# Kernel tuning notes

Hardware: AMD Instinct MI355X
Metric: run time of the kernel (lower is better)

The kernel has to match this reference:

```python
import jax, jax.numpy as jnp
import numpy as np

N, E, F_IN, HID, EDIM = 20000, 320000, 16, 64, 1


def _add_self_loops(src, dst, eattr, n):
    # PyG add_self_loops with fill_value='mean': self-loop edge_attr = mean of
    # incoming edge_attr per destination node (0 if no incoming edges).
    deg = jax.ops.segment_sum(jnp.ones_like(eattr[:, 0]), dst, num_segments=n)
    mean_attr = jax.ops.segment_sum(eattr, dst, num_segments=n) / jnp.maximum(deg, 1.0)[:, None]
    loop = jnp.arange(n)
    return (jnp.concatenate([src, loop]), jnp.concatenate([dst, loop]),
            jnp.concatenate([eattr, mean_attr], axis=0))


def _gat_layer(x, src, dst, eattr, W, a_src, a_dst, We, a_e, b, heads, out_ch, n):
    # shared linear for src/dst (PyG GATConv with int in_channels)
    h = (x @ W).reshape(n, heads, out_ch)                      # [N,H,C]
    al_s = jnp.einsum('nhc,hc->nh', h, a_src)                  # [N,H]
    al_d = jnp.einsum('nhc,hc->nh', h, a_dst)
    ef = (eattr @ We).reshape(-1, heads, out_ch)               # [E,H,C]
    al_e = jnp.einsum('ehc,hc->eh', ef, a_e)                   # [E,H]
    alpha = jax.nn.leaky_relu(al_s[src] + al_d[dst] + al_e, 0.2)
    # segment softmax over destination node
    m = jax.ops.segment_max(alpha, dst, num_segments=n)
    m = jnp.where(jnp.isfinite(m), m, 0.0)
    ex = jnp.exp(alpha - m[dst])
    den = jax.ops.segment_sum(ex, dst, num_segments=n)
    coef = ex / (den[dst] + 1e-16)                             # [E,H]
    out = jax.ops.segment_sum(h[src] * coef[:, :, None], dst, num_segments=n)
    return out.reshape(n, heads * out_ch) + b


def setup_inputs() -> dict:
    key = jax.random.key(0)
    ks = jax.random.split(key, 24)
    s = 0.1
    inp = {
        'x': jax.random.normal(ks[0], (N, F_IN), jnp.float32),
        'edge_index': jax.random.randint(ks[1], (2, E), 0, N, jnp.int64),
        'edge_attr': jax.random.uniform(ks[2], (E, EDIM), jnp.float32),
        # layer 0: heads=4, in=16, out=64
        'W0': jax.random.normal(ks[3], (F_IN, 4 * HID), jnp.float32) * s,
        'as0': jax.random.normal(ks[4], (4, HID), jnp.float32) * s,
        'ad0': jax.random.normal(ks[5], (4, HID), jnp.float32) * s,
        'We0': jax.random.normal(ks[6], (EDIM, 4 * HID), jnp.float32) * s,
        'ae0': jax.random.normal(ks[7], (4, HID), jnp.float32) * s,
        'b0': jnp.zeros((4 * HID,), jnp.float32),
        # layer 1: heads=4, in=256, out=64
        'W1': jax.random.normal(ks[8], (4 * HID, 4 * HID), jnp.float32) * s,
        'as1': jax.random.normal(ks[9], (4, HID), jnp.float32) * s,
        'ad1': jax.random.normal(ks[10], (4, HID), jnp.float32) * s,
        'We1': jax.random.normal(ks[11], (EDIM, 4 * HID), jnp.float32) * s,
        'ae1': jax.random.normal(ks[12], (4, HID), jnp.float32) * s,
        'b1': jnp.zeros((4 * HID,), jnp.float32),
        # layer 2: heads=1, in=256, out=64
        'W2': jax.random.normal(ks[13], (4 * HID, HID), jnp.float32) * s,
        'as2': jax.random.normal(ks[14], (1, HID), jnp.float32) * s,
        'ad2': jax.random.normal(ks[15], (1, HID), jnp.float32) * s,
        'We2': jax.random.normal(ks[16], (EDIM, HID), jnp.float32) * s,
        'ae2': jax.random.normal(ks[17], (1, HID), jnp.float32) * s,
        'b2': jnp.zeros((HID,), jnp.float32),
        'ln_g': jnp.ones((HID,), jnp.float32),
        'ln_b': jnp.zeros((HID,), jnp.float32),
    }
    return inp


def reference(x, edge_index, edge_attr,
              W0, as0, ad0, We0, ae0, b0,
              W1, as1, ad1, We1, ae1, b1,
              W2, as2, ad2, We2, ae2, b2,
              ln_g, ln_b):
    n = x.shape[0]
    src, dst, eattr = _add_self_loops(edge_index[0], edge_index[1], edge_attr, n)
    h = _gat_layer(x, src, dst, eattr, W0, as0, ad0, We0, ae0, b0, 4, HID, n)
    h = jax.nn.elu(h)  # dropout is identity in eval
    h = _gat_layer(h, src, dst, eattr, W1, as1, ad1, We1, ae1, b1, 4, HID, n)
    h = jax.nn.elu(h)
    h = _gat_layer(h, src, dst, eattr, W2, as2, ad2, We2, ae2, b2, 1, HID, n)
    mu = jnp.mean(h, axis=-1, keepdims=True)
    var = jnp.mean((h - mu) ** 2, axis=-1, keepdims=True)
    return (h - mu) / jnp.sqrt(var + 1e-5) * ln_g + ln_b
```

## Files before the change

kernel.cpp:

```cpp
#include <hip/hip_runtime.h>
#include <hip/hip_bf16.h>
#include <math.h>


typedef __attribute__((ext_vector_type(8))) short short8;
typedef __attribute__((ext_vector_type(4))) float float4v;

#define CAP 64

__device__ __forceinline__ float wave_sum(float v) {
#pragma unroll
  for (int off = 32; off > 0; off >>= 1) v += __shfl_xor(v, off, 64);
  return v;
}

__device__ __forceinline__ unsigned short f2bf(float v) {
  unsigned u = __float_as_uint(v);
  unsigned r = u + 0x7fff + ((u >> 16) & 1);
  return (unsigned short)(r >> 16);
}

__device__ __forceinline__ float bf2f(unsigned short u) {
  return __uint_as_float(((unsigned)u) << 16);
}

__global__ __launch_bounds__(256) void k1_kernel(
    const float* __restrict__ x, const int* __restrict__ srcv, const int* __restrict__ dstv,
    const float* __restrict__ eattr,
    const float* __restrict__ W0, const float* __restrict__ as0, const float* __restrict__ ad0,
    const float* __restrict__ We0, const float* __restrict__ ae0,
    const float* __restrict__ W1, const float* __restrict__ as1, const float* __restrict__ ad1,
    const float* __restrict__ We1, const float* __restrict__ ae1,
    const float* __restrict__ W2, const float* __restrict__ as2, const float* __restrict__ ad2,
    const float* __restrict__ We2, const float* __restrict__ ae2,
    unsigned short* __restrict__ Wf1, unsigned short* __restrict__ Wf2,
    float* __restrict__ wedot, float* __restrict__ al_s, float* __restrict__ al_d,
    int* __restrict__ deg, int2* __restrict__ ebuf,
    int N, int E, int gD) {
  int b = blockIdx.x;
  int tid = threadIdx.x;
  if (b < 272) {
    int idx = b * 256 + tid;
    int j = idx & 7, lane = (idx >> 3) & 63, ks = (idx >> 9) & 7, nt = idx >> 12;
    int k = ks * 32 + (lane >> 4) * 8 + j;
    int col = lane & 15;
    float v = 0.f;
    if (nt < 16) {
      v = W1[(size_t)k * 256 + nt * 16 + col];
    } else if (col < 4) {
      for (int c = 0; c < 64; c++) v = fmaf(W1[(size_t)k * 256 + col * 64 + c], as1[col * 64 + c], v);
    } else if (col < 8) {
      int h = col - 4;
      for (int c = 0; c < 64; c++) v = fmaf(W1[(size_t)k * 256 + h * 64 + c], ad1[h * 64 + c], v);
    }
    Wf1[idx] = f2bf(v);
  } else if (b < 352) {
    int idx = (b - 272) * 256 + tid;
    int j = idx & 7, lane = (idx >> 3) & 63, ks = (idx >> 9) & 7, nt = idx >> 12;
    int k = ks * 32 + (lane >> 4) * 8 + j;
    int col = lane & 15;
    float v = 0.f;
    if (nt < 4) {
      v = W2[(size_t)k * 64 + nt * 16 + col];
    } else if (col < 1) {
      for (int c = 0; c < 64; c++) v = fmaf(W2[(size_t)k * 64 + c], as2[c], v);
    } else if (col < 2) {
      for (int c = 0; c < 64; c++) v = fmaf(W2[(size_t)k * 64 + c], ad2[c], v);
    }
    Wf2[idx] = f2bf(v);
  } else if (b == 352) {
    if (tid >= 64) return;
    int c = tid;
    for (int h = 0; h < 4; h++) {
      float v = wave_sum(We0[h * 64 + c] * ae0[h * 64 + c]);
      if (c == 0) wedot[h] = v;
    }
    for (int h = 0; h < 4; h++) {
      float v = wave_sum(We1[h * 64 + c] * ae1[h * 64 + c]);
      if (c == 0) wedot[4 + h] = v;
    }
    float v = wave_sum(We2[c] * ae2[c]);
    if (c == 0) wedot[8] = v;
  } else if (b < 353 + gD) {
    __shared__ float va[128];
    if (tid < 128) {
      int k = tid >> 3, col = tid & 7;
      float v = 0.f;
      if (col < 4) {
        for (int c = 0; c < 64; c++) v = fmaf(W0[(size_t)k * 256 + col * 64 + c], as0[col * 64 + c], v);
      } else {
        int h = col - 4;
        for (int c = 0; c < 64; c++) v = fmaf(W0[(size_t)k * 256 + h * 64 + c], ad0[h * 64 + c], v);
      }
      va[tid] = v;
    }
    __syncthreads();
    int node = (b - 353) * 256 + tid;
    if (node >= N) return;
    const float4* xr = (const float4*)(x + (size_t)node * 16);
    float4 xv[4];
#pragma unroll
    for (int q = 0; q < 4; q++) xv[q] = xr[q];
    float al[8];
#pragma unroll
    for (int j = 0; j < 8; j++) al[j] = 0.f;
#pragma unroll
    for (int k = 0; k < 16; k++) {
      float xk = ((const float*)xv)[k];
#pragma unroll
      for (int j = 0; j < 8; j++) al[j] = fmaf(xk, va[k * 8 + j], al[j]);
    }
    ((float4*)al_s)[node] = make_float4(al[0], al[1], al[2], al[3]);
    ((float4*)al_d)[node] = make_float4(al[4], al[5], al[6], al[7]);
  } else {
    int e = (b - 353 - gD) * 256 + tid;
    if (e >= E) return;
    int d = dstv[e];
    int s = srcv[e];
    float ea = eattr[e];
    int pos = atomicAdd(&deg[d], 1);
    if (pos < CAP) ebuf[(size_t)d * CAP + pos] = make_int2(s, __float_as_int(ea));
  }
}

__global__ __launch_bounds__(256) void agg0_kernel(
    const int* __restrict__ deg, const int2* __restrict__ ebuf,
    const float* __restrict__ al_s, const float* __restrict__ al_d,
    const float* __restrict__ wedot,
    const float* __restrict__ x, const float* __restrict__ W0,
    const float* __restrict__ bias, unsigned short* __restrict__ out, int n) {
  int node = blockIdx.x * 4 + (threadIdx.x >> 6);
  if (node >= n) return;
  int lane = threadIdx.x & 63;
  int es = lane >> 4;
  int c = lane & 15;
  int dg = deg[node];
  int cnt = dg < CAP ? dg : CAP;
  float xself = x[(size_t)node * 16 + c];
  float4 as4s = ((const float4*)al_s)[node];
  float4 ald = ((const float4*)al_d)[node];
  float wd[4];
#pragma unroll
  for (int h = 0; h < 4; h++) wd[h] = wedot[h];

  float Z[4] = {0.f, 0.f, 0.f, 0.f};
  float den[4] = {0.f, 0.f, 0.f, 0.f};
  float easum = 0.f;

  for (int i = 0; i < cnt; i += 4) {
    int base = __builtin_amdgcn_readfirstlane(node * CAP + i);
    int2 r0 = ebuf[base], r1 = ebuf[base + 1], r2 = ebuf[base + 2], r3 = ebuf[base + 3];
    int2 rm = (es == 0) ? r0 : (es == 1) ? r1 : (es == 2) ? r2 : r3;
    bool valid = (i + es) < cnt;
    int src = valid ? rm.x : 0;
    float ev = valid ? __int_as_float(rm.y) : 0.f;
    float xv = x[(size_t)src * 16 + c];
    float4 as4 = ((const float4*)al_s)[src];
    easum += ev;
#pragma unroll
    for (int h = 0; h < 4; h++) {
      float a = ((const float*)&as4)[h] + ((const float*)&ald)[h] + ev * wd[h];
      a = fmaxf(a, 0.2f * a);
      a = fminf(a, 30.f);
      float wv = __expf(a);
      wv = valid ? wv : 0.f;
      den[h] += wv;
      Z[h] = fmaf(wv, xv, Z[h]);
    }
  }

#pragma unroll
  for (int h = 0; h < 4; h++) {
    Z[h] += __shfl_xor(Z[h], 16, 64);
    Z[h] += __shfl_xor(Z[h], 32, 64);
    den[h] += __shfl_xor(den[h], 16, 64);
    den[h] += __shfl_xor(den[h], 32, 64);
  }
  easum += __shfl_xor(easum, 16, 64);
  easum += __shfl_xor(easum, 32, 64);

  {
    float evs = easum / fmaxf((float)dg, 1.f);
#pragma unroll
    for (int h = 0; h < 4; h++) {
      float a = ((const float*)&as4s)[h] + ((const float*)&ald)[h] + evs * wd[h];
      a = fmaxf(a, 0.2f * a);
      a = fminf(a, 30.f);
      float wv = __expf(a);
      den[h] += wv;
      Z[h] = fmaf(wv, xself, Z[h]);
    }
  }

  int h = es;
  float zsel = (h == 0) ? Z[0] : (h == 1) ? Z[1] : (h == 2) ? Z[2] : Z[3];
  float dsel = (h == 0) ? den[0] : (h == 1) ? den[1] : (h == 2) ? den[2] : den[3];
  float zn = zsel / (dsel + 1e-16f);
  float4 w0r[16];
#pragma unroll
  for (int cc = 0; cc < 16; cc++) w0r[cc] = ((const float4*)(W0 + (size_t)cc * 256))[lane];
  float zc[16];
  int basel = lane & 48;
#pragma unroll
  for (int cc = 0; cc < 16; cc++) zc[cc] = __shfl(zn, basel + cc, 64);
  float o[4];
  float4 b4 = ((const float4*)bias)[lane];
#pragma unroll
  for (int jj = 0; jj < 4; jj++) o[jj] = ((const float*)&b4)[jj];
#pragma unroll
  for (int cc = 0; cc < 16; cc++) {
#pragma unroll
    for (int jj = 0; jj < 4; jj++) o[jj] = fmaf(zc[cc], ((const float*)&w0r[cc])[jj], o[jj]);
  }
  ushort4 o4;
  float ox = o[0] > 0.f ? o[0] : expm1f(o[0]);
  float oy = o[1] > 0.f ? o[1] : expm1f(o[1]);
  float oz = o[2] > 0.f ? o[2] : expm1f(o[2]);
  float ow = o[3] > 0.f ? o[3] : expm1f(o[3]);
  o4.x = f2bf(ox);
  o4.y = f2bf(oy);
  o4.z = f2bf(oz);
  o4.w = f2bf(ow);
  ((ushort4*)out)[(size_t)node * 64 + lane] = o4;
}

template <int M, int H>
__global__ __launch_bounds__(64) void mfma_gemm_dots(
    const unsigned short* __restrict__ Abf, const unsigned short* __restrict__ Wfrag,
    unsigned short* __restrict__ out, float* __restrict__ al_s, float* __restrict__ al_d,
    int n) {
  int lane = threadIdx.x;
  int row0 = blockIdx.x * 16;
  int m = lane & 15, q = lane >> 4;

  short8 afrag[8];
  int r = row0 + m;
  if (r < n) {
    const short8* arow = (const short8*)(Abf + (size_t)r * 256);
#pragma unroll
    for (int ks = 0; ks < 8; ks++) afrag[ks] = arow[ks * 4 + q];
  } else {
#pragma unroll
    for (int ks = 0; ks < 8; ks++) afrag[ks] = (short8)0;
  }

  const short8* wf = (const short8*)Wfrag;

  auto epi = [&](int tile, float4v acc) {
    int col = tile * 16 + m;
#pragma unroll
    for (int reg = 0; reg < 4; reg++) {
      int rr = row0 + q * 4 + reg;
      if (rr < n) out[(size_t)rr * M + col] = f2bf(acc[reg]);
    }
  };

  for (int nt = 0; nt < M / 16; nt += 2) {
    const short8* b0 = wf + (size_t)nt * 8 * 64 + lane;
    const short8* b1 = b0 + 8 * 64;
    short8 bf0[8], bf1[8];
#pragma unroll
    for (int ks = 0; ks < 8; ks++) {
      bf0[ks] = b0[ks * 64];
      bf1[ks] = b1[ks * 64];
    }
    float4v acc0 = {0.f, 0.f, 0.f, 0.f};
    float4v acc1 = {0.f, 0.f, 0.f, 0.f};
#pragma unroll
    for (int ks = 0; ks < 8; ks++) {
      acc0 = __builtin_amdgcn_mfma_f32_16x16x32_bf16(afrag[ks], bf0[ks], acc0, 0, 0, 0);
      acc1 = __builtin_amdgcn_mfma_f32_16x16x32_bf16(afrag[ks], bf1[ks], acc1, 0, 0, 0);
    }
    epi(nt, acc0);
    epi(nt + 1, acc1);
  }

  {
    const short8* bl = wf + (size_t)(M / 16) * 8 * 64 + lane;
    short8 bf[8];
#pragma unroll
    for (int ks = 0; ks < 8; ks++) bf[ks] = bl[ks * 64];
    float4v acc = {0.f, 0.f, 0.f, 0.f};
#pragma unroll
    for (int ks = 0; ks < 8; ks++)
      acc = __builtin_amdgcn_mfma_f32_16x16x32_bf16(afrag[ks], bf[ks], acc, 0, 0, 0);
#pragma unroll
    for (int reg = 0; reg < 4; reg++) {
      int rr = row0 + q * 4 + reg;
      if (rr < n) {
        if (m < H) al_s[(size_t)rr * H + m] = acc[reg];
        else if (m < 2 * H) al_d[(size_t)rr * H + (m - H)] = acc[reg];
      }
    }
  }
}

__global__ __launch_bounds__(256) void agg4_kernel(
    const int* __restrict__ deg, const int2* __restrict__ ebuf,
    const float* __restrict__ al_s, const float* __restrict__ al_d,
    const float* __restrict__ wedot,
    const unsigned short* __restrict__ B, const float* __restrict__ bias,
    unsigned short* __restrict__ out, int n) {
  int node = blockIdx.x * 4 + (threadIdx.x >> 6);
  if (node >= n) return;
  int lane = threadIdx.x & 63;
  int half = lane >> 5;
  int l = lane & 31;
  int h4 = l >> 3;
  int dg = deg[node];
  int cnt = dg < CAP ? dg : CAP;
  float aldh = al_d[(size_t)node * 4 + h4];
  float alsh = al_s[(size_t)node * 4 + h4];
  float wdh = wedot[h4];
  short8 rowS = ((const short8*)(B + (size_t)node * 256))[l];

  float acc[8];
#pragma unroll
  for (int j = 0; j < 8; j++) acc[j] = 0.f;
  float den = 0.f;
  float easum = 0.f;

  for (int i = 0; i < cnt; i += 4) {
    int base = __builtin_amdgcn_readfirstlane(node * CAP + i);
    int2 r0 = ebuf[base], r1 = ebuf[base + 1], r2 = ebuf[base + 2], r3 = ebuf[base + 3];
    bool vA = (i + (half ? 1 : 0)) < cnt;
    bool vB = (i + (half ? 3 : 2)) < cnt;
    int2 rA = half ? r1 : r0;
    int2 rB = half ? r3 : r2;
    int srcA = vA ? rA.x : 0;
    int srcB = vB ? rB.x : 0;
    float evA = vA ? __int_as_float(rA.y) : 0.f;
    float evB = vB ? __int_as_float(rB.y) : 0.f;
    easum += evA + evB;
    float aA = al_s[(size_t)srcA * 4 + h4] + aldh + evA * wdh;
    float aB = al_s[(size_t)srcB * 4 + h4] + aldh + evB * wdh;
    aA = fmaxf(aA, 0.2f * aA);
    aB = fmaxf(aB, 0.2f * aB);
    aA = fminf(aA, 30.f);
    aB = fminf(aB, 30.f);
    float wA = __expf(aA);
    float wB = __expf(aB);
    wA = vA ? wA : 0.f;
    wB = vB ? wB : 0.f;
    short8 rowA = ((const short8*)(B + (size_t)srcA * 256))[l];
    short8 rowB = ((const short8*)(B + (size_t)srcB * 256))[l];
    den += wA + wB;
    const unsigned short* pa = (const unsigned short*)&rowA;
    const unsigned short* pb = (const unsigned short*)&rowB;
#pragma unroll
    for (int j = 0; j < 8; j++) acc[j] = fmaf(wA, bf2f(pa[j]), acc[j]);
#pragma unroll
    for (int j = 0; j < 8; j++) acc[j] = fmaf(wB, bf2f(pb[j]), acc[j]);
  }

  den += __shfl_xor(den, 32, 64);
  easum += __shfl_xor(easum, 32, 64);
#pragma unroll
  for (int j = 0; j < 8; j++) acc[j] += __shfl_xor(acc[j], 32, 64);

  {
    float evs = easum / fmaxf((float)dg, 1.f);
    float a = alsh + aldh + evs * wdh;
    a = fmaxf(a, 0.2f * a);
    a = fminf(a, 30.f);
    float wv = __expf(a);
    const unsigned short* ps = (const unsigned short*)&rowS;
    den += wv;
#pragma unroll
    for (int j = 0; j < 8; j++) acc[j] = fmaf(wv, bf2f(ps[j]), acc[j]);
  }

  if (half == 0) {
    float inv = 1.f / (den + 1e-16f);
    float4 b0 = ((const float4*)bias)[l * 2];
    float4 b1 = ((const float4*)bias)[l * 2 + 1];
    unsigned short o8[8];
#pragma unroll
    for (int j = 0; j < 8; j++) {
      float bjv = (j < 4) ? ((const float*)&b0)[j] : ((const float*)&b1)[j - 4];
      float o = acc[j] * inv + bjv;
      o = o > 0.f ? o : expm1f(o);
      o8[j] = f2bf(o);
    }
    ((short8*)(out + (size_t)node * 256))[l] = *(short8*)o8;
  }
}

__global__ __launch_bounds__(256) void agg_ln_kernel(
    const int* __restrict__ deg, const int2* __restrict__ ebuf,
    const float* __restrict__ al_s, const float* __restrict__ al_d,
    const float* __restrict__ wedot,
    const unsigned short* __restrict__ B, const float* __restrict__ bias,
    const float* __restrict__ ln_g, const float* __restrict__ ln_b,
    float* __restrict__ out, int n) {
  int node = blockIdx.x * 4 + (threadIdx.x >> 6);
  if (node >= n) return;
  int lane = threadIdx.x & 63;
  int q = lane >> 4;
  int l = lane & 15;
  int dg = deg[node];
  int cnt = dg < CAP ? dg : CAP;
  float ald = al_d[node];
  float als = al_s[node];
  float wd = wedot[0];
  ushort4 bvS = ((const ushort4*)(B + (size_t)node * 64))[l];

  float4 acc = make_float4(0.f, 0.f, 0.f, 0.f);
  float den = 0.f;
  float easum = 0.f;

  for (int i = 0; i < cnt; i += 4) {
    int base = __builtin_amdgcn_readfirstlane(node * CAP + i);
    int2 r0 = ebuf[base], r1 = ebuf[base + 1], r2 = ebuf[base + 2], r3 = ebuf[base + 3];
    int2 rm = (q == 0) ? r0 : (q == 1) ? r1 : (q == 2) ? r2 : r3;
    bool valid = (i + q) < cnt;
    int src = valid ? rm.x : 0;
    float ev = valid ? __int_as_float(rm.y) : 0.f;
    easum += ev;
    float a = al_s[src] + ald + ev * wd;
    a = fmaxf(a, 0.2f * a);
    a = fminf(a, 30.f);
    float wv = __expf(a);
    wv = valid ? wv : 0.f;
    ushort4 bv = ((const ushort4*)(B + (size_t)src * 64))[l];
    den += wv;
    acc.x = fmaf(wv, bf2f(bv.x), acc.x);
    acc.y = fmaf(wv, bf2f(bv.y), acc.y);
    acc.z = fmaf(wv, bf2f(bv.z), acc.z);
    acc.w = fmaf(wv, bf2f(bv.w), acc.w);
  }

  den += __shfl_xor(den, 32, 64);
  den += __shfl_xor(den, 16, 64);
  easum += __shfl_xor(easum, 32, 64);
  easum += __shfl_xor(easum, 16, 64);
  acc.x += __shfl_xor(acc.x, 32, 64);
  acc.y += __shfl_xor(acc.y, 32, 64);
  acc.z += __shfl_xor(acc.z, 32, 64);
  acc.w += __shfl_xor(acc.w, 32, 64);
  acc.x += __shfl_xor(acc.x, 16, 64);
  acc.y += __shfl_xor(acc.y, 16, 64);
  acc.z += __shfl_xor(acc.z, 16, 64);
  acc.w += __shfl_xor(acc.w, 16, 64);

  {
    float evs = easum / fmaxf((float)dg, 1.f);
    float a = als + ald + evs * wd;
    a = fmaxf(a, 0.2f * a);
    a = fminf(a, 30.f);
    float wv = __expf(a);
    den += wv;
    acc.x = fmaf(wv, bf2f(bvS.x), acc.x);
    acc.y = fmaf(wv, bf2f(bvS.y), acc.y);
    acc.z = fmaf(wv, bf2f(bvS.z), acc.z);
    acc.w = fmaf(wv, bf2f(bvS.w), acc.w);
  }

  float inv = 1.f / (den + 1e-16f);
  float4 b4 = ((const float4*)bias)[l];
  float4 o;
  o.x = acc.x * inv + b4.x;
  o.y = acc.y * inv + b4.y;
  o.z = acc.z * inv + b4.z;
  o.w = acc.w * inv + b4.w;
  float s = (o.x + o.y) + (o.z + o.w);
#pragma unroll
  for (int off = 1; off < 16; off <<= 1) s += __shfl_xor(s, off, 64);
  float mu = s * (1.f / 64.f);
  float dx = o.x - mu, dy = o.y - mu, dz = o.z - mu, dw = o.w - mu;
  float v = (dx * dx + dy * dy) + (dz * dz + dw * dw);
#pragma unroll
  for (int off = 1; off < 16; off <<= 1) v += __shfl_xor(v, off, 64);
  float rs = rsqrtf(v * (1.f / 64.f) + 1e-5f);
  if (q == 0) {
    float4 g4 = ((const float4*)ln_g)[l];
    float4 lb4 = ((const float4*)ln_b)[l];
    float4 rr;
    rr.x = dx * rs * g4.x + lb4.x;
    rr.y = dy * rs * g4.y + lb4.y;
    rr.z = dz * rs * g4.z + lb4.z;
    rr.w = dw * rs * g4.w + lb4.w;
    ((float4*)(out + (size_t)node * 64))[l] = rr;
  }
}

extern "C" void kernel_launch(void* const* d_in, const int* in_sizes, int n_in,
                              void* d_out, int out_size, void* d_ws, size_t ws_size,
                              hipStream_t stream) {
  const float* x = (const float*)d_in[0];
  const int* ei = (const int*)d_in[1];
  const float* eattr = (const float*)d_in[2];
  const float* W0 = (const float*)d_in[3];
  const float* as0 = (const float*)d_in[4];
  const float* ad0 = (const float*)d_in[5];
  const float* We0 = (const float*)d_in[6];
  const float* ae0 = (const float*)d_in[7];
  const float* b0 = (const float*)d_in[8];
  const float* W1 = (const float*)d_in[9];
  const float* as1 = (const float*)d_in[10];
  const float* ad1 = (const float*)d_in[11];
  const float* We1 = (const float*)d_in[12];
  const float* ae1 = (const float*)d_in[13];
  const float* b1 = (const float*)d_in[14];
  const float* W2 = (const float*)d_in[15];
  const float* as2 = (const float*)d_in[16];
  const float* ad2 = (const float*)d_in[17];
  const float* We2 = (const float*)d_in[18];
  const float* ae2 = (const float*)d_in[19];
  const float* b2 = (const float*)d_in[20];
  const float* lng = (const float*)d_in[21];
  const float* lnb = (const float*)d_in[22];
  float* outp = (float*)d_out;

  const int N = in_sizes[0] / 16;
  const int E = in_sizes[1] / 2;
  const int* srcv = ei;
  const int* dstv = ei + E;

  char* w = (char*)d_ws;
  size_t off = 0;
  auto alloc = [&](size_t bytes) -> void* {
    void* p = w + off;
    off += (bytes + 255) & ~(size_t)255;
    return p;
  };
  int* deg = (int*)alloc((size_t)N * 4);
  size_t zero_bytes = off;
  int2* ebuf = (int2*)alloc(((size_t)N * CAP + 8) * 8);
  float* wedot = (float*)alloc(16 * 4);
  float* al_s = (float*)alloc((size_t)N * 4 * 4);
  float* al_d = (float*)alloc((size_t)N * 4 * 4);
  unsigned short* Wf1 = (unsigned short*)alloc((size_t)17 * 4096 * 2);
  unsigned short* Wf2 = (unsigned short*)alloc((size_t)5 * 4096 * 2);
  unsigned short* bufA = (unsigned short*)alloc((size_t)N * 256 * 2);
  unsigned short* bufB = (unsigned short*)alloc((size_t)N * 256 * 2);
  (void)ws_size;

  hipMemsetAsync(d_ws, 0, zero_bytes, stream);

  int gE = (E + 255) / 256;
  int gD = (N + 255) / 256;

  k1_kernel<<<353 + gD + gE, 256, 0, stream>>>(
      x, srcv, dstv, eattr, W0, as0, ad0, We0, ae0, W1, as1, ad1, We1, ae1,
      W2, as2, ad2, We2, ae2, Wf1, Wf2, wedot, al_s, al_d, deg, ebuf, N, E, gD);

  int gStrip = (N + 15) / 16;
  int gNode4 = (N + 3) / 4;

  agg0_kernel<<<gNode4, 256, 0, stream>>>(deg, ebuf, al_s, al_d, wedot, x, W0, b0,
                                          bufA, N);

  mfma_gemm_dots<256, 4><<<gStrip, 64, 0, stream>>>(bufA, Wf1, bufB, al_s, al_d, N);
  agg4_kernel<<<gNode4, 256, 0, stream>>>(deg, ebuf, al_s, al_d, wedot + 4, bufB, b1,
                                          bufA, N);

  mfma_gemm_dots<64, 1><<<gStrip, 64, 0, stream>>>(bufA, Wf2, bufB, al_s, al_d, N);
  agg_ln_kernel<<<gNode4, 256, 0, stream>>>(deg, ebuf, al_s, al_d, wedot + 8, bufB, b2,
                                            lng, lnb, outp, N);
}
```

Before: 215.1 us.

## Fuse per-layer aggregation with following MFMA GEMM through shared-memory row tiles

Each aggregation kernel now processes a 16-node tile: four waves each aggregate four nodes, write the bf16 activated rows into shared memory, then the block runs the next layer's MFMA projection (including the attention-dot columns) straight from LDS. This removes two kernel launches and the global write and re-read of the intermediate 256-wide activation buffer. It also gives each layer its own attention-score buffers so a fused kernel never overwrites scores it is still reading. In exchange, each block handles nodes serially per wave, which lowers parallelism and can add tail imbalance when degrees vary.

```diff
diff --git a/kernel.cpp b/kernel.cpp
--- a/kernel.cpp
+++ b/kernel.cpp
@@ -34,7 +34,7 @@
     const float* __restrict__ W2, const float* __restrict__ as2, const float* __restrict__ ad2,
     const float* __restrict__ We2, const float* __restrict__ ae2,
     unsigned short* __restrict__ Wf1, unsigned short* __restrict__ Wf2,
-    float* __restrict__ wedot, float* __restrict__ al_s, float* __restrict__ al_d,
+    float* __restrict__ wedot, float* __restrict__ al0s, float* __restrict__ al0d,
     int* __restrict__ deg, int2* __restrict__ ebuf,
     int N, int E, int gD) {
   int b = blockIdx.x;
@@ -110,8 +110,8 @@
 #pragma unroll
       for (int j = 0; j < 8; j++) al[j] = fmaf(xk, va[k * 8 + j], al[j]);
     }
-    ((float4*)al_s)[node] = make_float4(al[0], al[1], al[2], al[3]);
-    ((float4*)al_d)[node] = make_float4(al[4], al[5], al[6], al[7]);
+    ((float4*)al0s)[node] = make_float4(al[0], al[1], al[2], al[3]);
+    ((float4*)al0d)[node] = make_float4(al[4], al[5], al[6], al[7]);
   } else {
     int e = (b - 353 - gD) * 256 + tid;
     if (e >= E) return;
@@ -123,160 +123,128 @@
   }
 }
 
-__global__ __launch_bounds__(256) void agg0_kernel(
+__global__ __launch_bounds__(256) void fused0_kernel(
     const int* __restrict__ deg, const int2* __restrict__ ebuf,
-    const float* __restrict__ al_s, const float* __restrict__ al_d,
+    const float* __restrict__ al0s, const float* __restrict__ al0d,
     const float* __restrict__ wedot,
     const float* __restrict__ x, const float* __restrict__ W0,
-    const float* __restrict__ bias, unsigned short* __restrict__ out, int n) {
-  int node = blockIdx.x * 4 + (threadIdx.x >> 6);
-  if (node >= n) return;
+    const float* __restrict__ b0, const unsigned short* __restrict__ Wf1,
+    unsigned short* __restrict__ buf256, float* __restrict__ al1s,
+    float* __restrict__ al1d, int n) {
+  __shared__ unsigned short hrow[16][264];
+  int tile = blockIdx.x;
+  int wv = threadIdx.x >> 6;
   int lane = threadIdx.x & 63;
   int es = lane >> 4;
   int c = lane & 15;
-  int dg = deg[node];
-  int cnt = dg < CAP ? dg : CAP;
-  float xself = x[(size_t)node * 16 + c];
-  float4 as4s = ((const float4*)al_s)[node];
-  float4 ald = ((const float4*)al_d)[node];
-  float wd[4];
-#pragma unroll
-  for (int h = 0; h < 4; h++) wd[h] = wedot[h];
-
-  float Z[4] = {0.f, 0.f, 0.f, 0.f};
-  float den[4] = {0.f, 0.f, 0.f, 0.f};
-  float easum = 0.f;
-
-  for (int i = 0; i < cnt; i += 4) {
-    int base = __builtin_amdgcn_readfirstlane(node * CAP + i);
-    int2 r0 = ebuf[base], r1 = ebuf[base + 1], r2 = ebuf[base + 2], r3 = ebuf[base + 3];
-    int2 rm = (es == 0) ? r0 : (es == 1) ? r1 : (es == 2) ? r2 : r3;
-    bool valid = (i + es) < cnt;
-    int src = valid ? rm.x : 0;
-    float ev = valid ? __int_as_float(rm.y) : 0.f;
-    float xv = x[(size_t)src * 16 + c];
-    float4 as4 = ((const float4*)al_s)[src];
-    easum += ev;
-#pragma unroll
-    for (int h = 0; h < 4; h++) {
-      float a = ((const float*)&as4)[h] + ((const float*)&ald)[h] + ev * wd[h];
-      a = fmaxf(a, 0.2f * a);
-      a = fminf(a, 30.f);
-      float wv = __expf(a);
-      wv = valid ? wv : 0.f;
-      den[h] += wv;
-      Z[h] = fmaf(wv, xv, Z[h]);
-    }
-  }
-
-#pragma unroll
-  for (int h = 0; h < 4; h++) {
-    Z[h] += __shfl_xor(Z[h], 16, 64);
-    Z[h] += __shfl_xor(Z[h], 32, 64);
-    den[h] += __shfl_xor(den[h], 16, 64);
-    den[h] += __shfl_xor(den[h], 32, 64);
-  }
-  easum += __shfl_xor(easum, 16, 64);
-  easum += __shfl_xor(easum, 32, 64);
-
-  {
-    float evs = easum / fmaxf((float)dg, 1.f);
-#pragma unroll
-    for (int h = 0; h < 4; h++) {
-      float a = ((const float*)&as4s)[h] + ((const float*)&ald)[h] + evs * wd[h];
-      a = fmaxf(a, 0.2f * a);
-      a = fminf(a, 30.f);
-      float wv = __expf(a);
-      den[h] += wv;
-      Z[h] = fmaf(wv, xself, Z[h]);
-    }
-  }
-
-  int h = es;
-  float zsel = (h == 0) ? Z[0] : (h == 1) ? Z[1] : (h == 2) ? Z[2] : Z[3];
-  float dsel = (h == 0) ? den[0] : (h == 1) ? den[1] : (h == 2) ? den[2] : den[3];
-  float zn = zsel / (dsel + 1e-16f);
-  float4 w0r[16];
-#pragma unroll
-  for (int cc = 0; cc < 16; cc++) w0r[cc] = ((const float4*)(W0 + (size_t)cc * 256))[lane];
-  float zc[16];
-  int basel = lane & 48;
-#pragma unroll
-  for (int cc = 0; cc < 16; cc++) zc[cc] = __shfl(zn, basel + cc, 64);
-  float o[4];
-  float4 b4 = ((const float4*)bias)[lane];
-#pragma unroll
-  for (int jj = 0; jj < 4; jj++) o[jj] = ((const float*)&b4)[jj];
-#pragma unroll
-  for (int cc = 0; cc < 16; cc++) {
-#pragma unroll
-    for (int jj = 0; jj < 4; jj++) o[jj] = fmaf(zc[cc], ((const float*)&w0r[cc])[jj], o[jj]);
-  }
-  ushort4 o4;
-  float ox = o[0] > 0.f ? o[0] : expm1f(o[0]);
-  float oy = o[1] > 0.f ? o[1] : expm1f(o[1]);
-  float oz = o[2] > 0.f ? o[2] : expm1f(o[2]);
-  float ow = o[3] > 0.f ? o[3] : expm1f(o[3]);
-  o4.x = f2bf(ox);
-  o4.y = f2bf(oy);
-  o4.z = f2bf(oz);
-  o4.w = f2bf(ow);
-  ((ushort4*)out)[(size_t)node * 64 + lane] = o4;
-}
-
-template <int M, int H>
-__global__ __launch_bounds__(64) void mfma_gemm_dots(
-    const unsigned short* __restrict__ Abf, const unsigned short* __restrict__ Wfrag,
-    unsigned short* __restrict__ out, float* __restrict__ al_s, float* __restrict__ al_d,
-    int n) {
-  int lane = threadIdx.x;
-  int row0 = blockIdx.x * 16;
+
+  for (int s = 0; s < 4; s++) {
+    int r = wv * 4 + s;
+    int node = tile * 16 + r;
+    if (node < n) {
+      int dg = deg[node];
+      int cnt = dg < CAP ? dg : CAP;
+      float xself = x[(size_t)node * 16 + c];
+      float4 as4s = ((const float4*)al0s)[node];
+      float4 ald = ((const float4*)al0d)[node];
+      float wd[4];
+#pragma unroll
+      for (int h = 0; h < 4; h++) wd[h] = wedot[h];
+
+      float Z[4] = {0.f, 0.f, 0.f, 0.f};
+      float den[4] = {0.f, 0.f, 0.f, 0.f};
+      float easum = 0.f;
+
+      for (int i = 0; i < cnt; i += 4) {
+        int base = __builtin_amdgcn_readfirstlane(node * CAP + i);
+        int2 r0 = ebuf[base], r1 = ebuf[base + 1], r2 = ebuf[base + 2], r3 = ebuf[base + 3];
+        int2 rm = (es == 0) ? r0 : (es == 1) ? r1 : (es == 2) ? r2 : r3;
+        bool valid = (i + es) < cnt;
+        int src = valid ? rm.x : 0;
+        float ev = valid ? __int_as_float(rm.y) : 0.f;
+        float xv = x[(size_t)src * 16 + c];
+        float4 as4 = ((const float4*)al0s)[src];
+        easum += ev;
+#pragma unroll
+        for (int h = 0; h < 4; h++) {
+          float a = ((const float*)&as4)[h] + ((const float*)&ald)[h] + ev * wd[h];
+          a = fmaxf(a, 0.2f * a);
+          a = fminf(a, 30.f);
+          float wvv = __expf(a);
+          wvv = valid ? wvv : 0.f;
+          den[h] += wvv;
+          Z[h] = fmaf(wvv, xv, Z[h]);
+        }
+      }
+
+#pragma unroll
+      for (int h = 0; h < 4; h++) {
+        Z[h] += __shfl_xor(Z[h], 16, 64);
+        Z[h] += __shfl_xor(Z[h], 32, 64);
+        den[h] += __shfl_xor(den[h], 16, 64);
+        den[h] += __shfl_xor(den[h], 32, 64);
+      }
+      easum += __shfl_xor(easum, 16, 64);
+      easum += __shfl_xor(easum, 32, 64);
+
+      {
+        float evs = easum / fmaxf((float)dg, 1.f);
+#pragma unroll
+        for (int h = 0; h < 4; h++) {
+          float a = ((const float*)&as4s)[h] + ((const float*)&ald)[h] + evs * wd[h];
+          a = fmaxf(a, 0.2f * a);
+          a = fminf(a, 30.f);
+          float wvv = __expf(a);
+          den[h] += wvv;
+          Z[h] = fmaf(wvv, xself, Z[h]);
+        }
+      }
+
+      int h = es;
+      float zsel = (h == 0) ? Z[0] : (h == 1) ? Z[1] : (h == 2) ? Z[2] : Z[3];
+      float dsel = (h == 0) ? den[0] : (h == 1) ? den[1] : (h == 2) ? den[2] : den[3];
+      float zn = zsel / (dsel + 1e-16f);
+      float4 w0r[16];
+#pragma unroll
+      for (int cc = 0; cc < 16; cc++) w0r[cc] = ((const float4*)(W0 + (size_t)cc * 256))[lane];
+      float zc[16];
+      int basel = lane & 48;
+#pragma unroll
+      for (int cc = 0; cc < 16; cc++) zc[cc] = __shfl(zn, basel + cc, 64);
+      float o[4];
+      float4 b4 = ((const float4*)b0)[lane];
+#pragma unroll
+      for (int jj = 0; jj < 4; jj++) o[jj] = ((const float*)&b4)[jj];
+#pragma unroll
+      for (int cc = 0; cc < 16; cc++) {
+#pragma unroll
+        for (int jj = 0; jj < 4; jj++) o[jj] = fmaf(zc[cc], ((const float*)&w0r[cc])[jj], o[jj]);
+      }
+      ushort4 o4;
+      float ox = o[0] > 0.f ? o[0] : expm1f(o[0]);
+      float oy = o[1] > 0.f ? o[1] : expm1f(o[1]);
+      float oz = o[2] > 0.f ? o[2] : expm1f(o[2]);
+      float ow = o[3] > 0.f ? o[3] : expm1f(o[3]);
+      o4.x = f2bf(ox);
+      o4.y = f2bf(oy);
+      o4.z = f2bf(oz);
+      o4.w = f2bf(ow);
+      *(ushort4*)&hrow[r][lane * 4] = o4;
+    } else {
+      *(ushort4*)&hrow[r][lane * 4] = make_ushort4(0, 0, 0, 0);
+    }
+  }
+  __syncthreads();
+
   int m = lane & 15, q = lane >> 4;
-
+  int row0 = tile * 16;
   short8 afrag[8];
-  int r = row0 + m;
-  if (r < n) {
-    const short8* arow = (const short8*)(Abf + (size_t)r * 256);
-#pragma unroll
-    for (int ks = 0; ks < 8; ks++) afrag[ks] = arow[ks * 4 + q];
-  } else {
-#pragma unroll
-    for (int ks = 0; ks < 8; ks++) afrag[ks] = (short8)0;
-  }
-
-  const short8* wf = (const short8*)Wfrag;
-
-  auto epi = [&](int tile, float4v acc) {
-    int col = tile * 16 + m;
-#pragma unroll
-    for (int reg = 0; reg < 4; reg++) {
-      int rr = row0 + q * 4 + reg;
-      if (rr < n) out[(size_t)rr * M + col] = f2bf(acc[reg]);
-    }
-  };
-
-  for (int nt = 0; nt < M / 16; nt += 2) {
-    const short8* b0 = wf + (size_t)nt * 8 * 64 + lane;
-    const short8* b1 = b0 + 8 * 64;
-    short8 bf0[8], bf1[8];
-#pragma unroll
-    for (int ks = 0; ks < 8; ks++) {
-      bf0[ks] = b0[ks * 64];
-      bf1[ks] = b1[ks * 64];
-    }
-    float4v acc0 = {0.f, 0.f, 0.f, 0.f};
-    float4v acc1 = {0.f, 0.f, 0.f, 0.f};
-#pragma unroll
-    for (int ks = 0; ks < 8; ks++) {
-      acc0 = __builtin_amdgcn_mfma_f32_16x16x32_bf16(afrag[ks], bf0[ks], acc0, 0, 0, 0);
-      acc1 = __builtin_amdgcn_mfma_f32_16x16x32_bf16(afrag[ks], bf1[ks], acc1, 0, 0, 0);
-    }
-    epi(nt, acc0);
-    epi(nt + 1, acc1);
-  }
-
-  {
-    const short8* bl = wf + (size_t)(M / 16) * 8 * 64 + lane;
+#pragma unroll
+  for (int ks = 0; ks < 8; ks++) afrag[ks] = *(short8*)&hrow[m][ks * 32 + q * 8];
+
+  const short8* wf = (const short8*)Wf1;
+  for (int nt = wv; nt < 17; nt += 4) {
+    const short8* bl = wf + (size_t)nt * 8 * 64 + lane;
     short8 bf[8];
 #pragma unroll
     for (int ks = 0; ks < 8; ks++) bf[ks] = bl[ks * 64];
@@ -284,111 +252,168 @@
 #pragma unroll
     for (int ks = 0; ks < 8; ks++)
       acc = __builtin_amdgcn_mfma_f32_16x16x32_bf16(afrag[ks], bf[ks], acc, 0, 0, 0);
-#pragma unroll
-    for (int reg = 0; reg < 4; reg++) {
-      int rr = row0 + q * 4 + reg;
-      if (rr < n) {
-        if (m < H) al_s[(size_t)rr * H + m] = acc[reg];
-        else if (m < 2 * H) al_d[(size_t)rr * H + (m - H)] = acc[reg];
-      }
-    }
-  }
-}
-
-__global__ __launch_bounds__(256) void agg4_kernel(
+    if (nt < 16) {
+      int col = nt * 16 + m;
+#pragma unroll
+      for (int reg = 0; reg < 4; reg++) {
+        int rr = row0 + q * 4 + reg;
+        if (rr < n) buf256[(size_t)rr * 256 + col] = f2bf(acc[reg]);
+      }
+    } else {
+#pragma unroll
+      for (int reg = 0; reg < 4; reg++) {
+        int rr = row0 + q * 4 + reg;
+        if (rr < n) {
+          if (m < 4) al1s[(size_t)rr * 4 + m] = acc[reg];
+          else if (m < 8) al1d[(size_t)rr * 4 + (m - 4)] = acc[reg];
+        }
+      }
+    }
+  }
+}
+
+__global__ __launch_bounds__(256) void fused1_kernel(
     const int* __restrict__ deg, const int2* __restrict__ ebuf,
-    const float* __restrict__ al_s, const float* __restrict__ al_d,
+    const float* __restrict__ al1s, const float* __restrict__ al1d,
     const float* __restrict__ wedot,
-    const unsigned short* __restrict__ B, const float* __restrict__ bias,
-    unsigned short* __restrict__ out, int n) {
-  int node = blockIdx.x * 4 + (threadIdx.x >> 6);
-  if (node >= n) return;
+    const unsigned short* __restrict__ buf256, const float* __restrict__ b1,
+    const unsigned short* __restrict__ Wf2, unsigned short* __restrict__ buf64,
+    float* __restrict__ al2s, float* __restrict__ al2d, int n) {
+  __shared__ unsigned short hrow[16][264];
+  int tile = blockIdx.x;
+  int wv = threadIdx.x >> 6;
   int lane = threadIdx.x & 63;
   int half = lane >> 5;
   int l = lane & 31;
   int h4 = l >> 3;
-  int dg = deg[node];
-  int cnt = dg < CAP ? dg : CAP;
-  float aldh = al_d[(size_t)node * 4 + h4];
-  float alsh = al_s[(size_t)node * 4 + h4];
-  float wdh = wedot[h4];
-  short8 rowS = ((const short8*)(B + (size_t)node * 256))[l];
-
-  float acc[8];
-#pragma unroll
-  for (int j = 0; j < 8; j++) acc[j] = 0.f;
-  float den = 0.f;
-  float easum = 0.f;
-
-  for (int i = 0; i < cnt; i += 4) {
-    int base = __builtin_amdgcn_readfirstlane(node * CAP + i);
-    int2 r0 = ebuf[base], r1 = ebuf[base + 1], r2 = ebuf[base + 2], r3 = ebuf[base + 3];
-    bool vA = (i + (half ? 1 : 0)) < cnt;
-    bool vB = (i + (half ? 3 : 2)) < cnt;
-    int2 rA = half ? r1 : r0;
-    int2 rB = half ? r3 : r2;
-    int srcA = vA ? rA.x : 0;
-    int srcB = vB ? rB.x : 0;
-    float evA = vA ? __int_as_float(rA.y) : 0.f;
-    float evB = vB ? __int_as_float(rB.y) : 0.f;
-    easum += evA + evB;
-    float aA = al_s[(size_t)srcA * 4 + h4] + aldh + evA * wdh;
-    float aB = al_s[(size_t)srcB * 4 + h4] + aldh + evB * wdh;
-    aA = fmaxf(aA, 0.2f * aA);
-    aB = fmaxf(aB, 0.2f * aB);
-    aA = fminf(aA, 30.f);
-    aB = fminf(aB, 30.f);
-    float wA = __expf(aA);
-    float wB = __expf(aB);
-    wA = vA ? wA : 0.f;
-    wB = vB ? wB : 0.f;
-    short8 rowA = ((const short8*)(B + (size_t)srcA * 256))[l];
-    short8 rowB = ((const short8*)(B + (size_t)srcB * 256))[l];
-    den += wA + wB;
-    const unsigned short* pa = (const unsigned short*)&rowA;
-    const unsigned short* pb = (const unsigned short*)&rowB;
-#pragma unroll
-    for (int j = 0; j < 8; j++) acc[j] = fmaf(wA, bf2f(pa[j]), acc[j]);
-#pragma unroll
-    for (int j = 0; j < 8; j++) acc[j] = fmaf(wB, bf2f(pb[j]), acc[j]);
-  }
-
-  den += __shfl_xor(den, 32, 64);
-  easum += __shfl_xor(easum, 32, 64);
-#pragma unroll
-  for (int j = 0; j < 8; j++) acc[j] += __shfl_xor(acc[j], 32, 64);
-
-  {
-    float evs = easum / fmaxf((float)dg, 1.f);
-    float a = alsh + aldh + evs * wdh;
-    a = fmaxf(a, 0.2f * a);
-    a = fminf(a, 30.f);
-    float wv = __expf(a);
-    const unsigned short* ps = (const unsigned short*)&rowS;
-    den += wv;
-#pragma unroll
-    for (int j = 0; j < 8; j++) acc[j] = fmaf(wv, bf2f(ps[j]), acc[j]);
-  }
-
-  if (half == 0) {
-    float inv = 1.f / (den + 1e-16f);
-    float4 b0 = ((const float4*)bias)[l * 2];
-    float4 b1 = ((const float4*)bias)[l * 2 + 1];
-    unsigned short o8[8];
-#pragma unroll
-    for (int j = 0; j < 8; j++) {
-      float bjv = (j < 4) ? ((const float*)&b0)[j] : ((const float*)&b1)[j - 4];
-      float o = acc[j] * inv + bjv;
-      o = o > 0.f ? o : expm1f(o);
-      o8[j] = f2bf(o);
-    }
-    ((short8*)(out + (size_t)node * 256))[l] = *(short8*)o8;
+
+  for (int s = 0; s < 4; s++) {
+    int r = wv * 4 + s;
+    int node = tile * 16 + r;
+    if (node < n) {
+      int dg = deg[node];
+      int cnt = dg < CAP ? dg : CAP;
+      float aldh = al1d[(size_t)node * 4 + h4];
+      float alsh = al1s[(size_t)node * 4 + h4];
+      float wdh = wedot[4 + h4];
+      short8 rowS = ((const short8*)(buf256 + (size_t)node * 256))[l];
+
+      float acc[8];
+#pragma unroll
+      for (int j = 0; j < 8; j++) acc[j] = 0.f;
+      float den = 0.f;
+      float easum = 0.f;
+
+      for (int i = 0; i < cnt; i += 4) {
+        int base = __builtin_amdgcn_readfirstlane(node * CAP + i);
+        int2 r0 = ebuf[base], r1 = ebuf[base + 1], r2 = ebuf[base + 2], r3 = ebuf[base + 3];
+        bool vA = (i + (half ? 1 : 0)) < cnt;
+        bool vB = (i + (half ? 3 : 2)) < cnt;
+        int2 rA = half ? r1 : r0;
+        int2 rB = half ? r3 : r2;
+        int srcA = vA ? rA.x : 0;
+        int srcB = vB ? rB.x : 0;
+        float evA = vA ? __int_as_float(rA.y) : 0.f;
+        float evB = vB ? __int_as_float(rB.y) : 0.f;
+        easum += evA + evB;
+        float aA = al1s[(size_t)srcA * 4 + h4] + aldh + evA * wdh;
+        float aB = al1s[(size_t)srcB * 4 + h4] + aldh + evB * wdh;
+        aA = fmaxf(aA, 0.2f * aA);
+        aB = fmaxf(aB, 0.2f * aB);
+        aA = fminf(aA, 30.f);
+        aB = fminf(aB, 30.f);
+        float wA = __expf(aA);
+        float wB = __expf(aB);
+        wA = vA ? wA : 0.f;
+        wB = vB ? wB : 0.f;
+        short8 rowA = ((const short8*)(buf256 + (size_t)srcA * 256))[l];
+        short8 rowB = ((const short8*)(buf256 + (size_t)srcB * 256))[l];
+        den += wA + wB;
+        const unsigned short* pa = (const unsigned short*)&rowA;
+        const unsigned short* pb = (const unsigned short*)&rowB;
+#pragma unroll
+        for (int j = 0; j < 8; j++) acc[j] = fmaf(wA, bf2f(pa[j]), acc[j]);
+#pragma unroll
+        for (int j = 0; j < 8; j++) acc[j] = fmaf(wB, bf2f(pb[j]), acc[j]);
+      }
+
+      den += __shfl_xor(den, 32, 64);
+      easum += __shfl_xor(easum, 32, 64);
+#pragma unroll
+      for (int j = 0; j < 8; j++) acc[j] += __shfl_xor(acc[j], 32, 64);
+
+      {
+        float evs = easum / fmaxf((float)dg, 1.f);
+        float a = alsh + aldh + evs * wdh;
+        a = fmaxf(a, 0.2f * a);
+        a = fminf(a, 30.f);
+        float wvv = __expf(a);
+        const unsigned short* ps = (const unsigned short*)&rowS;
+        den += wvv;
+#pragma unroll
+        for (int j = 0; j < 8; j++) acc[j] = fmaf(wvv, bf2f(ps[j]), acc[j]);
+      }
+
+      if (half == 0) {
+        float inv = 1.f / (den + 1e-16f);
+        float4 bb0 = ((const float4*)b1)[l * 2];
+        float4 bb1 = ((const float4*)b1)[l * 2 + 1];
+        unsigned short o8[8];
+#pragma unroll
+        for (int j = 0; j < 8; j++) {
+          float bjv = (j < 4) ? ((const float*)&bb0)[j] : ((const float*)&bb1)[j - 4];
+          float o = acc[j] * inv + bjv;
+          o = o > 0.f ? o : expm1f(o);
+          o8[j] = f2bf(o);
+        }
+        *(short8*)&hrow[r][l * 8] = *(short8*)o8;
+      }
+    } else if (half == 0) {
+      unsigned short z8[8] = {0, 0, 0, 0, 0, 0, 0, 0};
+      *(short8*)&hrow[r][l * 8] = *(short8*)z8;
+    }
+  }
+  __syncthreads();
+
+  int m = lane & 15, q = lane >> 4;
+  int row0 = tile * 16;
+  short8 afrag[8];
+#pragma unroll
+  for (int ks = 0; ks < 8; ks++) afrag[ks] = *(short8*)&hrow[m][ks * 32 + q * 8];
+
+  const short8* wf = (const short8*)Wf2;
+  for (int nt = wv; nt < 5; nt += 4) {
+    const short8* bl = wf + (size_t)nt * 8 * 64 + lane;
+    short8 bf[8];
+#pragma unroll
+    for (int ks = 0; ks < 8; ks++) bf[ks] = bl[ks * 64];
+    float4v acc = {0.f, 0.f, 0.f, 0.f};
+#pragma unroll
+    for (int ks = 0; ks < 8; ks++)
+      acc = __builtin_amdgcn_mfma_f32_16x16x32_bf16(afrag[ks], bf[ks], acc, 0, 0, 0);
+    if (nt < 4) {
+      int col = nt * 16 + m;
+#pragma unroll
+      for (int reg = 0; reg < 4; reg++) {
+        int rr = row0 + q * 4 + reg;
+        if (rr < n) buf64[(size_t)rr * 64 + col] = f2bf(acc[reg]);
+      }
+    } else {
+#pragma unroll
+      for (int reg = 0; reg < 4; reg++) {
+        int rr = row0 + q * 4 + reg;
+        if (rr < n) {
+          if (m < 1) al2s[rr] = acc[reg];
+          else if (m < 2) al2d[rr] = acc[reg];
+        }
+      }
+    }
   }
 }
 
 __global__ __launch_bounds__(256) void agg_ln_kernel(
     const int* __restrict__ deg, const int2* __restrict__ ebuf,
-    const float* __restrict__ al_s, const float* __restrict__ al_d,
+    const float* __restrict__ al2s, const float* __restrict__ al2d,
     const float* __restrict__ wedot,
     const unsigned short* __restrict__ B, const float* __restrict__ bias,
     const float* __restrict__ ln_g, const float* __restrict__ ln_b,
@@ -400,8 +425,8 @@
   int l = lane & 15;
   int dg = deg[node];
   int cnt = dg < CAP ? dg : CAP;
-  float ald = al_d[node];
-  float als = al_s[node];
+  float ald = al2d[node];
+  float als = al2s[node];
   float wd = wedot[0];
   ushort4 bvS = ((const ushort4*)(B + (size_t)node * 64))[l];
 
@@ -417,7 +442,7 @@
     int src = valid ? rm.x : 0;
     float ev = valid ? __int_as_float(rm.y) : 0.f;
     easum += ev;
-    float a = al_s[src] + ald + ev * wd;
+    float a = al2s[src] + ald + ev * wd;
     a = fmaxf(a, 0.2f * a);
     a = fminf(a, 30.f);
     float wv = __expf(a);
@@ -528,12 +553,16 @@
   size_t zero_bytes = off;
   int2* ebuf = (int2*)alloc(((size_t)N * CAP + 8) * 8);
   float* wedot = (float*)alloc(16 * 4);
-  float* al_s = (float*)alloc((size_t)N * 4 * 4);
-  float* al_d = (float*)alloc((size_t)N * 4 * 4);
+  float* al0s = (float*)alloc((size_t)N * 4 * 4);
+  float* al0d = (float*)alloc((size_t)N * 4 * 4);
+  float* al1s = (float*)alloc((size_t)N * 4 * 4);
+  float* al1d = (float*)alloc((size_t)N * 4 * 4);
+  float* al2s = (float*)alloc((size_t)N * 4);
+  float* al2d = (float*)alloc((size_t)N * 4);
   unsigned short* Wf1 = (unsigned short*)alloc((size_t)17 * 4096 * 2);
   unsigned short* Wf2 = (unsigned short*)alloc((size_t)5 * 4096 * 2);
-  unsigned short* bufA = (unsigned short*)alloc((size_t)N * 256 * 2);
-  unsigned short* bufB = (unsigned short*)alloc((size_t)N * 256 * 2);
+  unsigned short* buf256 = (unsigned short*)alloc((size_t)N * 256 * 2);
+  unsigned short* buf64 = (unsigned short*)alloc((size_t)N * 64 * 2);
   (void)ws_size;
 
   hipMemsetAsync(d_ws, 0, zero_bytes, stream);
@@ -543,19 +572,17 @@
 
   k1_kernel<<<353 + gD + gE, 256, 0, stream>>>(
       x, srcv, dstv, eattr, W0, as0, ad0, We0, ae0, W1, as1, ad1, We1, ae1,
-      W2, as2, ad2, We2, ae2, Wf1, Wf2, wedot, al_s, al_d, deg, ebuf, N, E, gD);
-
-  int gStrip = (N + 15) / 16;
+      W2, as2, ad2, We2, ae2, Wf1, Wf2, wedot, al0s, al0d, deg, ebuf, N, E, gD);
+
+  int gT = (N + 15) / 16;
   int gNode4 = (N + 3) / 4;
 
-  agg0_kernel<<<gNode4, 256, 0, stream>>>(deg, ebuf, al_s, al_d, wedot, x, W0, b0,
-                                          bufA, N);
-
-  mfma_gemm_dots<256, 4><<<gStrip, 64, 0, stream>>>(bufA, Wf1, bufB, al_s, al_d, N);
-  agg4_kernel<<<gNode4, 256, 0, stream>>>(deg, ebuf, al_s, al_d, wedot + 4, bufB, b1,
-                                          bufA, N);
-
-  mfma_gemm_dots<64, 1><<<gStrip, 64, 0, stream>>>(bufA, Wf2, bufB, al_s, al_d, N);
-  agg_ln_kernel<<<gNode4, 256, 0, stream>>>(deg, ebuf, al_s, al_d, wedot + 8, bufB, b2,
-                                            lng, lnb, outp, N);
-}
+  fused0_kernel<<<gT, 256, 0, stream>>>(deg, ebuf, al0s, al0d, wedot, x, W0, b0,
+                                        Wf1, buf256, al1s, al1d, N);
+
+  fused1_kernel<<<gT, 256, 0, stream>>>(deg, ebuf, al1s, al1d, wedot, buf256, b1,
+                                        Wf2, buf64, al2s, al2d, N);
+
+  agg_ln_kernel<<<gNode4, 256, 0, stream>>>(deg, ebuf, al2s, al2d, wedot + 8,
+                                            buf64, b2, lng, lnb, outp, N);
+}
```

Result: no change. 214.6 us (-0.2%).
